# Kernel tuning notes

Hardware: AMD Instinct MI355X
Metric: run time of the kernel (lower is better)

The kernel has to match this reference:

```python
import jax, jax.numpy as jnp
import numpy as np

DIAG_MASK = 1e20  # value added on the diagonal to exclude self as negative


def setup_inputs() -> dict:
    key = jax.random.key(0)
    k1, k2, k3 = jax.random.split(key, 3)
    B, D_in, D_out = 4096, 1024, 1024
    anchor_x = jax.random.normal(k1, (B, D_in), dtype=jnp.float32)
    pos_x = jax.random.normal(k2, (B, D_in), dtype=jnp.float32)
    W = jax.random.normal(k3, (D_in, D_out), dtype=jnp.float32) * (1.0 / np.sqrt(D_in))
    b = jnp.zeros((D_out,), dtype=jnp.float32)
    return {"anchor_x": anchor_x, "pos_x": pos_x, "W": W, "b": b}


def reference(anchor_x, pos_x, W, b):
    # Encoder: simple dense projection (stand-in for the wrapped BERT encoder).
    anchor = anchor_x @ W + b          # [B, D]
    pos = pos_x @ W + b                # [B, D]

    # Pairwise squared distances dist[i,j] = ||anchor_i - pos_j||^2,
    # computed via the GEMM identity |a|^2 + |p|^2 - 2 a.p (same math as the
    # original broadcasted (a_i - p_j)^2 reduce_sum, far less memory traffic).
    a2 = jnp.sum(anchor * anchor, axis=-1, keepdims=True)       # [B, 1]
    p2 = jnp.sum(pos * pos, axis=-1, keepdims=True).T           # [1, B]
    dist = a2 + p2 - 2.0 * (anchor @ pos.T)                     # [B, B]

    B = dist.shape[0]
    mask_dist = dist + jnp.eye(B, dtype=dist.dtype) * DIAG_MASK  # mask diagonal
    indices = jnp.argmin(mask_dist, axis=-1)                     # [B] hard negatives
    neg = pos[indices]                                           # gather [B, D]

    return jnp.concatenate([anchor, pos, neg], axis=-1)          # [B, 3D]
```

## Files before the change

kernel.cpp:

```cpp
#include <hip/hip_runtime.h>


typedef short s8v __attribute__((ext_vector_type(8)));
typedef float f4v __attribute__((ext_vector_type(4)));
typedef unsigned short u16;

#define B  4096
#define D  1024
#define OLD 3072
#define OLD16 6144
#define LDK 68

__device__ __forceinline__ u16 f2bf(float f) {
  union { float f; unsigned u; } v; v.f = f;
  unsigned r = v.u + 0x7FFFu + ((v.u >> 16) & 1u);
  return (u16)(r >> 16);
}
__device__ __forceinline__ float bf2f(u16 s) {
  union { unsigned u; float f; } v; v.u = ((unsigned)s) << 16;
  return v.f;
}

__device__ __forceinline__ void gld16(const void* g, void* l) {
  __builtin_amdgcn_global_load_lds(
      (const __attribute__((address_space(1))) unsigned int*)g,
      (__attribute__((address_space(3))) unsigned int*)l, 16, 0, 0);
}

struct Top2 { float v1, v2; int j1, j2; };
__device__ __forceinline__ void t2_insert(Top2& t, float v, int j) {
  if (v < t.v1 || (v == t.v1 && j < t.j1)) {
    t.v2 = t.v1; t.j2 = t.j1; t.v1 = v; t.j1 = j;
  } else if (v < t.v2 || (v == t.v2 && j < t.j2)) {
    t.v2 = v; t.j2 = j;
  }
}

__global__ void splitT_W(const float* __restrict__ W, u16* __restrict__ WtQ) {
  __shared__ float tile[32][33];
  const int bx = blockIdx.x * 32, by = blockIdx.y * 32;
  const int tx = threadIdx.x, ty = threadIdx.y;
  for (int dy = 0; dy < 32; dy += 8)
    tile[ty + dy][tx] = W[(size_t)(by + ty + dy) * D + bx + tx];
  __syncthreads();
  for (int dy = 0; dy < 32; dy += 8) {
    const float v = tile[tx][ty + dy];
    const u16 h = f2bf(v);
    const size_t o = (size_t)(bx + ty + dy) * 2048 + by + tx;
    WtQ[o] = h;
    WtQ[o + 1024] = f2bf(v - bf2f(h));
  }
}

__global__ __launch_bounds__(256) void splitX(const float* __restrict__ X,
                                              u16* __restrict__ O16) {
  const int r = blockIdx.x, t = threadIdx.x;
  const float4 v = *(const float4*)&X[(size_t)r * D + t * 4];
  const float vv[4] = {v.x, v.y, v.z, v.w};
  ushort4 hi, mi;
  u16* hp = &hi.x; u16* mp = &mi.x;
#pragma unroll
  for (int i = 0; i < 4; ++i) {
    hp[i] = f2bf(vv[i]);
    mp[i] = f2bf(vv[i] - bf2f(hp[i]));
  }
  *(ushort4*)&O16[(size_t)r * OLD16 + 4096 + t * 4] = hi;
  *(ushort4*)&O16[(size_t)r * OLD16 + 5120 + t * 4] = mi;
}

__global__ __launch_bounds__(256) void enc_mfma(
    float* out ,
    const u16* __restrict__ WtQ, const float* __restrict__ bias, int outOff,
    u16* __restrict__ Q) {
  __shared__ __align__(16) u16 lAh[128 * 32], lAm[128 * 32];
  __shared__ __align__(16) u16 lBh[128 * 32], lBm[128 * 32];
  const u16* O16 = (const u16*)out;
  const int tid = threadIdx.x, lane = tid & 63, wave = tid >> 6;
  const int waveM = wave >> 1, waveN = wave & 1;
  const int row16 = lane & 15, quad = lane >> 4;
  const int Mbase = blockIdx.y * 128;
  const int Nbase = blockIdx.x * 128;
  f4v acc[4][4] = {};

  for (int kk = 0; kk < D; kk += 32) {
    __syncthreads();
#pragma unroll
    for (int i = 0; i < 2; ++i) {
      const int c = i * 256 + wave * 64 + lane;
      const int row = c >> 2, col8 = (c & 3) * 8;
      const int lo = (i * 256 + wave * 64) * 8;
      gld16(&O16[(size_t)(Mbase + row) * OLD16 + 4096 + kk + col8], &lAh[lo]);
      gld16(&O16[(size_t)(Mbase + row) * OLD16 + 5120 + kk + col8], &lAm[lo]);
      gld16(&WtQ[(size_t)(Nbase + row) * 2048 + kk + col8], &lBh[lo]);
      gld16(&WtQ[(size_t)(Nbase + row) * 2048 + 1024 + kk + col8], &lBm[lo]);
    }
    __syncthreads();
    s8v ah[4], am[4], bh[4], bm[4];
#pragma unroll
    for (int mi = 0; mi < 4; ++mi) {
      const int ro = (waveM * 64 + mi * 16 + row16) * 32 + quad * 8;
      ah[mi] = *(const s8v*)&lAh[ro];
      am[mi] = *(const s8v*)&lAm[ro];
    }
#pragma unroll
    for (int ni = 0; ni < 4; ++ni) {
      const int ro = (waveN * 64 + ni * 16 + row16) * 32 + quad * 8;
      bh[ni] = *(const s8v*)&lBh[ro];
      bm[ni] = *(const s8v*)&lBm[ro];
    }
#pragma unroll
    for (int mi = 0; mi < 4; ++mi)
#pragma unroll
      for (int ni = 0; ni < 4; ++ni) {
        f4v a = acc[mi][ni];
        a = __builtin_amdgcn_mfma_f32_16x16x32_bf16(ah[mi], bh[ni], a, 0, 0, 0);
        a = __builtin_amdgcn_mfma_f32_16x16x32_bf16(ah[mi], bm[ni], a, 0, 0, 0);
        a = __builtin_amdgcn_mfma_f32_16x16x32_bf16(am[mi], bh[ni], a, 0, 0, 0);
        acc[mi][ni] = a;
      }
  }
#pragma unroll
  for (int ni = 0; ni < 4; ++ni) {
    const int col = Nbase + waveN * 64 + ni * 16 + row16;
    const float bv = bias[col];
#pragma unroll
    for (int mi = 0; mi < 4; ++mi) {
      const int rbase = Mbase + waveM * 64 + mi * 16 + quad * 4;
#pragma unroll
      for (int r = 0; r < 4; ++r) {
        const size_t row = rbase + r;
        const float v = acc[mi][ni][r] + bv;
        out[row * OLD + outOff + col] = v;
        const u16 h = f2bf(v);
        Q[row * 2048 + col] = h;
        Q[row * 2048 + 1024 + col] = f2bf(v - bf2f(h));
      }
    }
  }
}

__global__ __launch_bounds__(256) void pnorm(float* __restrict__ o) {
  const int row = blockIdx.x, t = threadIdx.x;
  const float4 v = *(const float4*)&o[(size_t)row * OLD + D + t * 4];
  float s = v.x * v.x + v.y * v.y + v.z * v.z + v.w * v.w;
#pragma unroll
  for (int off = 32; off; off >>= 1) s += __shfl_down(s, off, 64);
  __shared__ float wsum[4];
  if ((t & 63) == 0) wsum[t >> 6] = s;
  __syncthreads();
  if (t == 0) o[(size_t)row * OLD + 2048] = wsum[0] + wsum[1] + wsum[2] + wsum[3];
}

__global__ __launch_bounds__(256) void dist_mfma(
    const u16* __restrict__ Aq, const u16* __restrict__ Pq, float* __restrict__ o) {
  __shared__ __align__(16) u16 lA[2][128 * 32];
  __shared__ __align__(16) u16 lB[2][128 * 32];
  __shared__ float sv1[128][2], sv2[128][2];
  __shared__ int sj1[128][2], sj2[128][2];
  const int tid = threadIdx.x, lane = tid & 63, wave = tid >> 6;
  const int waveM = wave >> 1, waveN = wave & 1;
  const int row16 = lane & 15, quad = lane >> 4;
  const int Mbase = blockIdx.y * 128;
  const int Nbase = blockIdx.x * 128;
  f4v acc[4][4] = {};

  for (int kk = 0; kk < D; kk += 32) {
    __syncthreads();
#pragma unroll
    for (int s = 0; s < 2; ++s) {
#pragma unroll
      for (int i = 0; i < 2; ++i) {
        const int c = i * 256 + wave * 64 + lane;
        const int row = c >> 2, col8 = (c & 3) * 8;
        const int lo = (i * 256 + wave * 64) * 8;
        gld16(&Aq[(size_t)(Mbase + row) * 2048 + s * 1024 + kk + col8], &lA[s][lo]);
        gld16(&Pq[(size_t)(Nbase + row) * 2048 + s * 1024 + kk + col8], &lB[s][lo]);
      }
    }
    __syncthreads();
    s8v ah[4], am[4], bh[4], bm[4];
#pragma unroll
    for (int i = 0; i < 4; ++i) {
      const int aro = (waveM * 64 + i * 16 + row16) * 32 + quad * 8;
      const int bro = (waveN * 64 + i * 16 + row16) * 32 + quad * 8;
      ah[i] = *(const s8v*)&lA[0][aro];
      am[i] = *(const s8v*)&lA[1][aro];
      bh[i] = *(const s8v*)&lB[0][bro];
      bm[i] = *(const s8v*)&lB[1][bro];
    }
#pragma unroll
    for (int mi = 0; mi < 4; ++mi)
#pragma unroll
      for (int ni = 0; ni < 4; ++ni) {
        f4v a = acc[mi][ni];
        a = __builtin_amdgcn_mfma_f32_16x16x32_bf16(ah[mi], bh[ni], a, 0, 0, 0);
        a = __builtin_amdgcn_mfma_f32_16x16x32_bf16(ah[mi], bm[ni], a, 0, 0, 0);
        a = __builtin_amdgcn_mfma_f32_16x16x32_bf16(am[mi], bh[ni], a, 0, 0, 0);
        acc[mi][ni] = a;
      }
  }

  float p2c[4];
#pragma unroll
  for (int ni = 0; ni < 4; ++ni)
    p2c[ni] = o[(size_t)(Nbase + waveN * 64 + ni * 16 + row16) * OLD + 2048];
#pragma unroll
  for (int mi = 0; mi < 4; ++mi)
#pragma unroll
    for (int r = 0; r < 4; ++r) {
      const int rg = Mbase + waveM * 64 + mi * 16 + quad * 4 + r;
      Top2 tp; tp.v1 = 3.0e38f; tp.v2 = 3.0e38f; tp.j1 = 0; tp.j2 = 1;
#pragma unroll
      for (int ni = 0; ni < 4; ++ni) {
        const int cg = Nbase + waveN * 64 + ni * 16 + row16;
        if (cg != rg) t2_insert(tp, p2c[ni] - 2.0f * acc[mi][ni][r], cg);
      }
#pragma unroll
      for (int m = 1; m < 16; m <<= 1) {
        const float ov1 = __shfl_xor(tp.v1, m, 64);
        const int oj1 = __shfl_xor(tp.j1, m, 64);
        const float ov2 = __shfl_xor(tp.v2, m, 64);
        const int oj2 = __shfl_xor(tp.j2, m, 64);
        t2_insert(tp, ov1, oj1);
        t2_insert(tp, ov2, oj2);
      }
      if (row16 == 0) {
        const int rl = waveM * 64 + mi * 16 + quad * 4 + r;
        sv1[rl][waveN] = tp.v1; sj1[rl][waveN] = tp.j1;
        sv2[rl][waveN] = tp.v2; sj2[rl][waveN] = tp.j2;
      }
    }
  __syncthreads();
  if (tid < 128) {
    Top2 tp; tp.v1 = sv1[tid][0]; tp.j1 = sj1[tid][0];
    tp.v2 = sv2[tid][0]; tp.j2 = sj2[tid][0];
    t2_insert(tp, sv1[tid][1], sj1[tid][1]);
    t2_insert(tp, sv2[tid][1], sj2[tid][1]);
    ((float4*)&o[(size_t)(Mbase + tid) * OLD + 2056])[blockIdx.x] =
        make_float4(tp.v1, __int_as_float(tp.j1), tp.v2, __int_as_float(tp.j2));
  }
}

__global__ __launch_bounds__(256) void argmin_refine(float* __restrict__ o) {
  const int i = blockIdx.x, t = threadIdx.x;
  __shared__ int gj[2];
  if (t < 32) {
    const float4 p = ((const float4*)&o[(size_t)i * OLD + 2056])[t];
    Top2 tp; tp.v1 = p.x; tp.j1 = __float_as_int(p.y);
    tp.v2 = p.z; tp.j2 = __float_as_int(p.w);
#pragma unroll
    for (int m = 1; m < 32; m <<= 1) {
      const float ov1 = __shfl_xor(tp.v1, m, 64);
      const int oj1 = __shfl_xor(tp.j1, m, 64);
      const float ov2 = __shfl_xor(tp.v2, m, 64);
      const int oj2 = __shfl_xor(tp.j2, m, 64);
      t2_insert(tp, ov1, oj1);
      t2_insert(tp, ov2, oj2);
    }
    if (t == 0) {
      gj[0] = (tp.j1 < 0) ? 0 : (tp.j1 > B - 1 ? B - 1 : tp.j1);
      gj[1] = (tp.j2 < 0) ? 0 : (tp.j2 > B - 1 ? B - 1 : tp.j2);
    }
  }
  __syncthreads();
  const int j1 = gj[0], j2 = gj[1];
  const float4 a4 = *(const float4*)&o[(size_t)i * OLD + t * 4];
  const float4 q1 = *(const float4*)&o[(size_t)j1 * OLD + D + t * 4];
  const float4 q2 = *(const float4*)&o[(size_t)j2 * OLD + D + t * 4];
  float s1 = a4.x * q1.x + a4.y * q1.y + a4.z * q1.z + a4.w * q1.w;
  float s2 = a4.x * q2.x + a4.y * q2.y + a4.z * q2.z + a4.w * q2.w;
  float n1 = q1.x * q1.x + q1.y * q1.y + q1.z * q1.z + q1.w * q1.w;
  float n2 = q2.x * q2.x + q2.y * q2.y + q2.z * q2.z + q2.w * q2.w;
#pragma unroll
  for (int off = 32; off; off >>= 1) {
    s1 += __shfl_down(s1, off, 64);
    s2 += __shfl_down(s2, off, 64);
    n1 += __shfl_down(n1, off, 64);
    n2 += __shfl_down(n2, off, 64);
  }
  __shared__ float wsum[4][4];
  __shared__ int sjf;
  if ((t & 63) == 0) {
    wsum[t >> 6][0] = s1; wsum[t >> 6][1] = s2;
    wsum[t >> 6][2] = n1; wsum[t >> 6][3] = n2;
  }
  __syncthreads();
  if (t == 0) {
    const float S1 = wsum[0][0] + wsum[1][0] + wsum[2][0] + wsum[3][0];
    const float S2 = wsum[0][1] + wsum[1][1] + wsum[2][1] + wsum[3][1];
    const float N1 = wsum[0][2] + wsum[1][2] + wsum[2][2] + wsum[3][2];
    const float N2 = wsum[0][3] + wsum[1][3] + wsum[2][3] + wsum[3][3];
    const float d1 = N1 - 2.0f * S1, d2 = N2 - 2.0f * S2;
    sjf = (d2 < d1 || (d2 == d1 && j2 < j1)) ? j2 : j1;
  }
  __syncthreads();
  const int j = sjf;
  ((float4*)&o[(size_t)i * OLD + 2048])[t] = ((const float4*)&o[(size_t)j * OLD + D])[t];
}

__global__ __launch_bounds__(256) void enc_gemm(
    const float* __restrict__ X, const float* __restrict__ W,
    const float* __restrict__ bia, float* __restrict__ out, int outOff) {
  __shared__ float lA[32][LDK];
  __shared__ float lW[32][LDK];
  const int tid = threadIdx.x;
  const int Mbase = blockIdx.y * 64;
  const int Nbase = blockIdx.x * 64;
  const int ty = tid >> 4, tx = tid & 15;
  float acc[4][4] = {};
  for (int k0 = 0; k0 < D; k0 += 32) {
    __syncthreads();
#pragma unroll
    for (int h = 0; h < 2; ++h) {
      const int ch = tid + h * 256;
      const int r = ch >> 3, c4 = (ch & 7) * 4;
      const float4 a4 = *(const float4*)&X[(size_t)(Mbase + r) * D + k0 + c4];
      lA[c4 + 0][r] = a4.x; lA[c4 + 1][r] = a4.y;
      lA[c4 + 2][r] = a4.z; lA[c4 + 3][r] = a4.w;
      const int kr = ch >> 4, nc = (ch & 15) * 4;
      *(float4*)&lW[kr][nc] = *(const float4*)&W[(size_t)(k0 + kr) * D + Nbase + nc];
    }
    __syncthreads();
#pragma unroll
    for (int kk = 0; kk < 32; ++kk) {
      const float4 av = *(const float4*)&lA[kk][ty * 4];
      const float4 wv = *(const float4*)&lW[kk][tx * 4];
      acc[0][0] += av.x * wv.x; acc[0][1] += av.x * wv.y; acc[0][2] += av.x * wv.z; acc[0][3] += av.x * wv.w;
      acc[1][0] += av.y * wv.x; acc[1][1] += av.y * wv.y; acc[1][2] += av.y * wv.z; acc[1][3] += av.y * wv.w;
      acc[2][0] += av.z * wv.x; acc[2][1] += av.z * wv.y; acc[2][2] += av.z * wv.z; acc[2][3] += av.z * wv.w;
      acc[3][0] += av.w * wv.x; acc[3][1] += av.w * wv.y; acc[3][2] += av.w * wv.z; acc[3][3] += av.w * wv.w;
    }
  }
  const float4 b4 = *(const float4*)&bia[Nbase + tx * 4];
#pragma unroll
  for (int i = 0; i < 4; ++i) {
    const int row = Mbase + ty * 4 + i;
    float4 ov;
    ov.x = acc[i][0] + b4.x; ov.y = acc[i][1] + b4.y;
    ov.z = acc[i][2] + b4.z; ov.w = acc[i][3] + b4.w;
    *(float4*)&out[(size_t)row * OLD + outOff + Nbase + tx * 4] = ov;
  }
}

__global__ __launch_bounds__(256) void dist_argmin_f32(float* __restrict__ o) {
  __shared__ float lA[32][LDK];
  __shared__ float lB[32][LDK];
  const int tid = threadIdx.x;
  const int Mbase = blockIdx.y * 64, Nbase = blockIdx.x * 64;
  const int ty = tid >> 4, tx = tid & 15;
  float acc[4][4] = {};
  for (int k0 = 0; k0 < D; k0 += 32) {
    __syncthreads();
#pragma unroll
    for (int h = 0; h < 2; ++h) {
      const int ch = tid + h * 256;
      const int r = ch >> 3, c4 = (ch & 7) * 4;
      const float4 a4 = *(const float4*)&o[(size_t)(Mbase + r) * OLD + k0 + c4];
      const float4 b4 = *(const float4*)&o[(size_t)(Nbase + r) * OLD + D + k0 + c4];
      lA[c4 + 0][r] = a4.x; lA[c4 + 1][r] = a4.y;
      lA[c4 + 2][r] = a4.z; lA[c4 + 3][r] = a4.w;
      lB[c4 + 0][r] = b4.x; lB[c4 + 1][r] = b4.y;
      lB[c4 + 2][r] = b4.z; lB[c4 + 3][r] = b4.w;
    }
    __syncthreads();
#pragma unroll
    for (int kk = 0; kk < 32; ++kk) {
      const float4 av = *(const float4*)&lA[kk][ty * 4];
      const float4 bv = *(const float4*)&lB[kk][tx * 4];
      acc[0][0] += av.x * bv.x; acc[0][1] += av.x * bv.y; acc[0][2] += av.x * bv.z; acc[0][3] += av.x * bv.w;
      acc[1][0] += av.y * bv.x; acc[1][1] += av.y * bv.y; acc[1][2] += av.y * bv.z; acc[1][3] += av.y * bv.w;
      acc[2][0] += av.z * bv.x; acc[2][1] += av.z * bv.y; acc[2][2] += av.z * bv.z; acc[2][3] += av.z * bv.w;
      acc[3][0] += av.w * bv.x; acc[3][1] += av.w * bv.y; acc[3][2] += av.w * bv.z; acc[3][3] += av.w * bv.w;
    }
  }
  float colp2[4];
#pragma unroll
  for (int j = 0; j < 4; ++j)
    colp2[j] = o[(size_t)(Nbase + tx * 4 + j) * OLD + 2048];
#pragma unroll
  for (int i = 0; i < 4; ++i) {
    const int rg = Mbase + ty * 4 + i;
    float bv = 3.0e38f; int bj = 0;
#pragma unroll
    for (int j = 0; j < 4; ++j) {
      const int cg = Nbase + tx * 4 + j;
      const float d = colp2[j] - 2.0f * acc[i][j];
      if (cg != rg && d < bv) { bv = d; bj = cg; }
    }
#pragma unroll
    for (int m = 1; m < 16; m <<= 1) {
      const float ov = __shfl_xor(bv, m, 64);
      const int oj = __shfl_xor(bj, m, 64);
      if (ov < bv || (ov == bv && oj < bj)) { bv = ov; bj = oj; }
    }
    if (tx == 0)
      ((float2*)&o[(size_t)rg * OLD + 2056])[blockIdx.x] =
          make_float2(bv, __int_as_float(bj));
  }
}

__global__ __launch_bounds__(256) void argmin_final_f2(float* __restrict__ o, int nblk) {
  const int i = blockIdx.x, t = threadIdx.x;
  __shared__ int sj;
  if (t < 64) {
    float v = 3.4e38f; int j = 0x7fffffff;
    if (t < nblk) {
      const float2 p = ((const float2*)&o[(size_t)i * OLD + 2056])[t];
      v = p.x; j = __float_as_int(p.y);
    }
#pragma unroll
    for (int m = 32; m; m >>= 1) {
      const float ov = __shfl_xor(v, m, 64);
      const int oj = __shfl_xor(j, m, 64);
      if (ov < v || (ov == v && oj < j)) { v = ov; j = oj; }
    }
    if (t == 0) sj = (j < 0) ? 0 : (j > B - 1 ? B - 1 : j);
  }
  __syncthreads();
  const int j = sj;
  ((float4*)&o[(size_t)i * OLD + 2048])[t] = ((const float4*)&o[(size_t)j * OLD + D])[t];
}

extern "C" void kernel_launch(void* const* d_in, const int* in_sizes, int n_in,
                              void* d_out, int out_size, void* d_ws, size_t ws_size,
                              hipStream_t stream) {
  const float* anchor_x = (const float*)d_in[0];
  const float* pos_x    = (const float*)d_in[1];
  const float* W        = (const float*)d_in[2];
  const float* b        = (const float*)d_in[3];
  float* out = (float*)d_out;
  char* ws = (char*)d_ws;
  const size_t MB = 1024 * 1024;

  if (ws_size >= 52 * MB) {
    u16* Aq  = (u16*)(ws);
    u16* Pq  = (u16*)(ws + 16 * MB);
    u16* WtQ = (u16*)(ws + 32 * MB);
    splitT_W<<<dim3(32, 32), dim3(32, 8), 0, stream>>>(W, WtQ);
    splitX<<<B, 256, 0, stream>>>(anchor_x, (u16*)out);
    enc_mfma<<<dim3(8, 32), 256, 0, stream>>>(out, WtQ, b, 0, Aq);
    splitX<<<B, 256, 0, stream>>>(pos_x, (u16*)out);
    enc_mfma<<<dim3(8, 32), 256, 0, stream>>>(out, WtQ, b, 1024, Pq);
    pnorm<<<B, 256, 0, stream>>>(out);
    dist_mfma<<<dim3(32, 32), 256, 0, stream>>>(Aq, Pq, out);
    argmin_refine<<<B, 256, 0, stream>>>(out);
  } else {
    enc_gemm<<<dim3(16, 64), 256, 0, stream>>>(anchor_x, W, b, out, 0);
    enc_gemm<<<dim3(16, 64), 256, 0, stream>>>(pos_x,    W, b, out, 1024);
    pnorm<<<B, 256, 0, stream>>>(out);
    dist_argmin_f32<<<dim3(64, 64), 256, 0, stream>>>(out);
    argmin_final_f2<<<B, 256, 0, stream>>>(out, 64);
  }
}
```

Measured before the change: 348.7 us.

## Merge anchor/pos encoder launches, drop one split-bf16 term, widen argmin refine to top-4

The anchor and positive input splits and encoder GEMMs are merged into single launches, with the positive bf16 split stored in a separate workspace region. This doubles the grid and removes two launches and the serialization between them. The distance GEMM drops the Ah×Pm cross term, cutting its MFMA count and LDS/global traffic by a third. The coarser distance values are compensated by keeping a top-4 candidate list per row instead of top-2 and re-ranking the candidates in fp32 during refinement. The risk is an argmin mismatch if the true minimum falls outside the top-4 of the approximate distances.

```diff
diff --git a/kernel.cpp b/kernel.cpp
--- a/kernel.cpp
+++ b/kernel.cpp
@@ -35,6 +35,19 @@
     t.v2 = v; t.j2 = j;
   }
 }
+struct Top4 { float v[4]; int j[4]; };
+__device__ __forceinline__ void t4_insert(Top4& t, float v, int j) {
+  if (v < t.v[3] || (v == t.v[3] && j < t.j[3])) {
+    int p = 3;
+#pragma unroll
+    for (int s = 0; s < 3; ++s) {
+      if (p > 0 && (v < t.v[p - 1] || (v == t.v[p - 1] && j < t.j[p - 1]))) {
+        t.v[p] = t.v[p - 1]; t.j[p] = t.j[p - 1]; --p;
+      }
+    }
+    t.v[p] = v; t.j[p] = j;
+  }
+}
 
 __global__ void splitT_W(const float* __restrict__ W, u16* __restrict__ WtQ) {
   __shared__ float tile[32][33];
@@ -52,10 +65,13 @@
   }
 }
 
-__global__ __launch_bounds__(256) void splitX(const float* __restrict__ X,
-                                              u16* __restrict__ O16) {
+__global__ __launch_bounds__(256) void splitX2(
+    const float* __restrict__ A, const float* __restrict__ P,
+    u16* __restrict__ O16, u16* __restrict__ posXq) {
   const int r = blockIdx.x, t = threadIdx.x;
-  const float4 v = *(const float4*)&X[(size_t)r * D + t * 4];
+  const bool isPos = r >= B;
+  const int row = isPos ? r - B : r;
+  const float4 v = *(const float4*)&(isPos ? P : A)[(size_t)row * D + t * 4];
   const float vv[4] = {v.x, v.y, v.z, v.w};
   ushort4 hi, mi;
   u16* hp = &hi.x; u16* mp = &mi.x;
@@ -64,21 +80,26 @@
     hp[i] = f2bf(vv[i]);
     mp[i] = f2bf(vv[i] - bf2f(hp[i]));
   }
-  *(ushort4*)&O16[(size_t)r * OLD16 + 4096 + t * 4] = hi;
-  *(ushort4*)&O16[(size_t)r * OLD16 + 5120 + t * 4] = mi;
+  if (isPos) {
+    *(ushort4*)&posXq[(size_t)row * 2048 + t * 4] = hi;
+    *(ushort4*)&posXq[(size_t)row * 2048 + 1024 + t * 4] = mi;
+  } else {
+    *(ushort4*)&O16[(size_t)row * OLD16 + 4096 + t * 4] = hi;
+    *(ushort4*)&O16[(size_t)row * OLD16 + 5120 + t * 4] = mi;
+  }
 }
 
 __global__ __launch_bounds__(256) void enc_mfma(
-    float* out ,
-    const u16* __restrict__ WtQ, const float* __restrict__ bias, int outOff,
-    u16* __restrict__ Q) {
+    float* out, const u16* __restrict__ posXq, const u16* __restrict__ WtQ,
+    const float* __restrict__ bias, u16* __restrict__ Aq, u16* __restrict__ Pq) {
   __shared__ __align__(16) u16 lAh[128 * 32], lAm[128 * 32];
   __shared__ __align__(16) u16 lBh[128 * 32], lBm[128 * 32];
   const u16* O16 = (const u16*)out;
   const int tid = threadIdx.x, lane = tid & 63, wave = tid >> 6;
   const int waveM = wave >> 1, waveN = wave & 1;
   const int row16 = lane & 15, quad = lane >> 4;
-  const int Mbase = blockIdx.y * 128;
+  const bool isPos = blockIdx.y >= 32;
+  const int Mbase = (blockIdx.y & 31) * 128;
   const int Nbase = blockIdx.x * 128;
   f4v acc[4][4] = {};
 
@@ -89,8 +110,13 @@
       const int c = i * 256 + wave * 64 + lane;
       const int row = c >> 2, col8 = (c & 3) * 8;
       const int lo = (i * 256 + wave * 64) * 8;
-      gld16(&O16[(size_t)(Mbase + row) * OLD16 + 4096 + kk + col8], &lAh[lo]);
-      gld16(&O16[(size_t)(Mbase + row) * OLD16 + 5120 + kk + col8], &lAm[lo]);
+      if (isPos) {
+        gld16(&posXq[(size_t)(Mbase + row) * 2048 + kk + col8], &lAh[lo]);
+        gld16(&posXq[(size_t)(Mbase + row) * 2048 + 1024 + kk + col8], &lAm[lo]);
+      } else {
+        gld16(&O16[(size_t)(Mbase + row) * OLD16 + 4096 + kk + col8], &lAh[lo]);
+        gld16(&O16[(size_t)(Mbase + row) * OLD16 + 5120 + kk + col8], &lAm[lo]);
+      }
       gld16(&WtQ[(size_t)(Nbase + row) * 2048 + kk + col8], &lBh[lo]);
       gld16(&WtQ[(size_t)(Nbase + row) * 2048 + 1024 + kk + col8], &lBm[lo]);
     }
@@ -119,6 +145,8 @@
         acc[mi][ni] = a;
       }
   }
+  const int outOff = isPos ? 1024 : 0;
+  u16* Q = isPos ? Pq : Aq;
 #pragma unroll
   for (int ni = 0; ni < 4; ++ni) {
     const int col = Nbase + waveN * 64 + ni * 16 + row16;
@@ -153,8 +181,8 @@
 
 __global__ __launch_bounds__(256) void dist_mfma(
     const u16* __restrict__ Aq, const u16* __restrict__ Pq, float* __restrict__ o) {
-  __shared__ __align__(16) u16 lA[2][128 * 32];
-  __shared__ __align__(16) u16 lB[2][128 * 32];
+  __shared__ __align__(16) u16 lAh[128 * 32], lAm[128 * 32];
+  __shared__ __align__(16) u16 lBh[128 * 32];
   __shared__ float sv1[128][2], sv2[128][2];
   __shared__ int sj1[128][2], sj2[128][2];
   const int tid = threadIdx.x, lane = tid & 63, wave = tid >> 6;
@@ -167,26 +195,23 @@
   for (int kk = 0; kk < D; kk += 32) {
     __syncthreads();
 #pragma unroll
-    for (int s = 0; s < 2; ++s) {
-#pragma unroll
-      for (int i = 0; i < 2; ++i) {
-        const int c = i * 256 + wave * 64 + lane;
-        const int row = c >> 2, col8 = (c & 3) * 8;
-        const int lo = (i * 256 + wave * 64) * 8;
-        gld16(&Aq[(size_t)(Mbase + row) * 2048 + s * 1024 + kk + col8], &lA[s][lo]);
-        gld16(&Pq[(size_t)(Nbase + row) * 2048 + s * 1024 + kk + col8], &lB[s][lo]);
-      }
-    }
-    __syncthreads();
-    s8v ah[4], am[4], bh[4], bm[4];
+    for (int i = 0; i < 2; ++i) {
+      const int c = i * 256 + wave * 64 + lane;
+      const int row = c >> 2, col8 = (c & 3) * 8;
+      const int lo = (i * 256 + wave * 64) * 8;
+      gld16(&Aq[(size_t)(Mbase + row) * 2048 + kk + col8], &lAh[lo]);
+      gld16(&Aq[(size_t)(Mbase + row) * 2048 + 1024 + kk + col8], &lAm[lo]);
+      gld16(&Pq[(size_t)(Nbase + row) * 2048 + kk + col8], &lBh[lo]);
+    }
+    __syncthreads();
+    s8v ah[4], am[4], bh[4];
 #pragma unroll
     for (int i = 0; i < 4; ++i) {
       const int aro = (waveM * 64 + i * 16 + row16) * 32 + quad * 8;
       const int bro = (waveN * 64 + i * 16 + row16) * 32 + quad * 8;
-      ah[i] = *(const s8v*)&lA[0][aro];
-      am[i] = *(const s8v*)&lA[1][aro];
-      bh[i] = *(const s8v*)&lB[0][bro];
-      bm[i] = *(const s8v*)&lB[1][bro];
+      ah[i] = *(const s8v*)&lAh[aro];
+      am[i] = *(const s8v*)&lAm[aro];
+      bh[i] = *(const s8v*)&lBh[bro];
     }
 #pragma unroll
     for (int mi = 0; mi < 4; ++mi)
@@ -194,7 +219,6 @@
       for (int ni = 0; ni < 4; ++ni) {
         f4v a = acc[mi][ni];
         a = __builtin_amdgcn_mfma_f32_16x16x32_bf16(ah[mi], bh[ni], a, 0, 0, 0);
-        a = __builtin_amdgcn_mfma_f32_16x16x32_bf16(ah[mi], bm[ni], a, 0, 0, 0);
         a = __builtin_amdgcn_mfma_f32_16x16x32_bf16(am[mi], bh[ni], a, 0, 0, 0);
         acc[mi][ni] = a;
       }
@@ -243,55 +267,70 @@
 
 __global__ __launch_bounds__(256) void argmin_refine(float* __restrict__ o) {
   const int i = blockIdx.x, t = threadIdx.x;
-  __shared__ int gj[2];
-  if (t < 32) {
-    const float4 p = ((const float4*)&o[(size_t)i * OLD + 2056])[t];
-    Top2 tp; tp.v1 = p.x; tp.j1 = __float_as_int(p.y);
-    tp.v2 = p.z; tp.j2 = __float_as_int(p.w);
+  __shared__ int gj[4];
+  if (t < 64) {
+    Top4 tp;
+#pragma unroll
+    for (int c = 0; c < 4; ++c) { tp.v[c] = 3.0e38f; tp.j[c] = 0; }
+    if (t < 32) {
+      const float4 p = ((const float4*)&o[(size_t)i * OLD + 2056])[t];
+      t4_insert(tp, p.x, __float_as_int(p.y));
+      t4_insert(tp, p.z, __float_as_int(p.w));
+    }
 #pragma unroll
     for (int m = 1; m < 32; m <<= 1) {
-      const float ov1 = __shfl_xor(tp.v1, m, 64);
-      const int oj1 = __shfl_xor(tp.j1, m, 64);
-      const float ov2 = __shfl_xor(tp.v2, m, 64);
-      const int oj2 = __shfl_xor(tp.j2, m, 64);
-      t2_insert(tp, ov1, oj1);
-      t2_insert(tp, ov2, oj2);
+#pragma unroll
+      for (int c = 0; c < 4; ++c) {
+        const float ov = __shfl_xor(tp.v[c], m, 64);
+        const int oj = __shfl_xor(tp.j[c], m, 64);
+        t4_insert(tp, ov, oj);
+      }
     }
     if (t == 0) {
-      gj[0] = (tp.j1 < 0) ? 0 : (tp.j1 > B - 1 ? B - 1 : tp.j1);
-      gj[1] = (tp.j2 < 0) ? 0 : (tp.j2 > B - 1 ? B - 1 : tp.j2);
-    }
-  }
-  __syncthreads();
-  const int j1 = gj[0], j2 = gj[1];
+#pragma unroll
+      for (int c = 0; c < 4; ++c)
+        gj[c] = (tp.j[c] < 0) ? 0 : (tp.j[c] > B - 1 ? B - 1 : tp.j[c]);
+    }
+  }
+  __syncthreads();
+  int jj[4];
+#pragma unroll
+  for (int c = 0; c < 4; ++c) jj[c] = gj[c];
   const float4 a4 = *(const float4*)&o[(size_t)i * OLD + t * 4];
-  const float4 q1 = *(const float4*)&o[(size_t)j1 * OLD + D + t * 4];
-  const float4 q2 = *(const float4*)&o[(size_t)j2 * OLD + D + t * 4];
-  float s1 = a4.x * q1.x + a4.y * q1.y + a4.z * q1.z + a4.w * q1.w;
-  float s2 = a4.x * q2.x + a4.y * q2.y + a4.z * q2.z + a4.w * q2.w;
-  float n1 = q1.x * q1.x + q1.y * q1.y + q1.z * q1.z + q1.w * q1.w;
-  float n2 = q2.x * q2.x + q2.y * q2.y + q2.z * q2.z + q2.w * q2.w;
-#pragma unroll
-  for (int off = 32; off; off >>= 1) {
-    s1 += __shfl_down(s1, off, 64);
-    s2 += __shfl_down(s2, off, 64);
-    n1 += __shfl_down(n1, off, 64);
-    n2 += __shfl_down(n2, off, 64);
-  }
-  __shared__ float wsum[4][4];
+  float s[4], n[4];
+#pragma unroll
+  for (int c = 0; c < 4; ++c) {
+    const float4 q = *(const float4*)&o[(size_t)jj[c] * OLD + D + t * 4];
+    s[c] = a4.x * q.x + a4.y * q.y + a4.z * q.z + a4.w * q.w;
+    n[c] = q.x * q.x + q.y * q.y + q.z * q.z + q.w * q.w;
+  }
+#pragma unroll
+  for (int off = 32; off; off >>= 1)
+#pragma unroll
+    for (int c = 0; c < 4; ++c) {
+      s[c] += __shfl_down(s[c], off, 64);
+      n[c] += __shfl_down(n[c], off, 64);
+    }
+  __shared__ float wsum[4][8];
   __shared__ int sjf;
-  if ((t & 63) == 0) {
-    wsum[t >> 6][0] = s1; wsum[t >> 6][1] = s2;
-    wsum[t >> 6][2] = n1; wsum[t >> 6][3] = n2;
-  }
+  if ((t & 63) == 0)
+#pragma unroll
+    for (int c = 0; c < 4; ++c) {
+      wsum[t >> 6][c] = s[c];
+      wsum[t >> 6][4 + c] = n[c];
+    }
   __syncthreads();
   if (t == 0) {
-    const float S1 = wsum[0][0] + wsum[1][0] + wsum[2][0] + wsum[3][0];
-    const float S2 = wsum[0][1] + wsum[1][1] + wsum[2][1] + wsum[3][1];
-    const float N1 = wsum[0][2] + wsum[1][2] + wsum[2][2] + wsum[3][2];
-    const float N2 = wsum[0][3] + wsum[1][3] + wsum[2][3] + wsum[3][3];
-    const float d1 = N1 - 2.0f * S1, d2 = N2 - 2.0f * S2;
-    sjf = (d2 < d1 || (d2 == d1 && j2 < j1)) ? j2 : j1;
+    float bd = 3.4e38f; int bj = 0x7fffffff;
+#pragma unroll
+    for (int c = 0; c < 4; ++c) {
+      const float S = wsum[0][c] + wsum[1][c] + wsum[2][c] + wsum[3][c];
+      const float N = wsum[0][4 + c] + wsum[1][4 + c] + wsum[2][4 + c] + wsum[3][4 + c];
+      const float d = N - 2.0f * S;
+      const int j = jj[c];
+      if (d < bd || (d == bd && j < bj)) { bd = d; bj = j; }
+    }
+    sjf = bj;
   }
   __syncthreads();
   const int j = sjf;
@@ -433,14 +472,13 @@
   const size_t MB = 1024 * 1024;
 
   if (ws_size >= 52 * MB) {
-    u16* Aq  = (u16*)(ws);
-    u16* Pq  = (u16*)(ws + 16 * MB);
-    u16* WtQ = (u16*)(ws + 32 * MB);
+    u16* Aq     = (u16*)(ws);
+    u16* Pq     = (u16*)(ws + 16 * MB);
+    u16* WtQ    = (u16*)(ws + 32 * MB);
+    u16* posXq  = (u16*)(ws + 36 * MB);
     splitT_W<<<dim3(32, 32), dim3(32, 8), 0, stream>>>(W, WtQ);
-    splitX<<<B, 256, 0, stream>>>(anchor_x, (u16*)out);
-    enc_mfma<<<dim3(8, 32), 256, 0, stream>>>(out, WtQ, b, 0, Aq);
-    splitX<<<B, 256, 0, stream>>>(pos_x, (u16*)out);
-    enc_mfma<<<dim3(8, 32), 256, 0, stream>>>(out, WtQ, b, 1024, Pq);
+    splitX2<<<2 * B, 256, 0, stream>>>(anchor_x, pos_x, (u16*)out, posXq);
+    enc_mfma<<<dim3(8, 64), 256, 0, stream>>>(out, posXq, WtQ, b, Aq, Pq);
     pnorm<<<B, 256, 0, stream>>>(out);
     dist_mfma<<<dim3(32, 32), 256, 0, stream>>>(Aq, Pq, out);
     argmin_refine<<<B, 256, 0, stream>>>(out);
```

Result: faster. 336.3 us (-3.6%).
